# Kernel tuning notes

Measured on AMD Instinct MI355X. Metric: run time of the kernel, lower is better.

## Reference

```python
import jax, jax.numpy as jnp
import numpy as np

B, NM, MB, D = 16, 64, 64, 1024
NH, NKV, MEM = 16, 8, 64
HD = D // NH            # 64
S = MB + MEM            # per-step attention length
EPS = 1e-6

def precompute_freqs_cis(dim, end, theta=10000.0):
    freqs = 1.0 / (theta ** (jnp.arange(0, dim, 2)[: dim // 2].astype(jnp.float32) / dim))
    t = jnp.arange(end, dtype=jnp.float32)
    return jnp.exp(1j * jnp.outer(t, freqs))  # [end, dim//2] complex64

def apply_rope(x, fcis):
    # x: [s, h, d], fcis: [s, d//2] complex
    xc = x.reshape(x.shape[0], x.shape[1], HD // 2, 2)
    xc = jax.lax.complex(xc[..., 0], xc[..., 1]) * fcis[:, None, :]
    return jnp.stack([jnp.real(xc), jnp.imag(xc)], axis=-1).reshape(x.shape)

def layer_norm(x, scale, bias):
    m = x.mean(-1, keepdims=True)
    v = x.var(-1, keepdims=True)
    return (x - m) * jax.lax.rsqrt(v + EPS) * scale + bias

def setup_inputs() -> dict:
    key = jax.random.key(0)
    ks = jax.random.split(key, 8)
    s = 1.0 / np.sqrt(D)
    return {
        'hidden_states': jax.random.normal(ks[0], (B, NM, MB, D), jnp.float32),
        'mask': jax.random.bernoulli(ks[1], 0.9, (B, NM)),
        'mem_state': jax.random.normal(ks[2], (MEM, D), jnp.float32) * s,
        'wq': jax.random.normal(ks[3], (D, D), jnp.float32) * s,
        'wk': jax.random.normal(ks[4], (D, NKV * HD), jnp.float32) * s,
        'wv': jax.random.normal(ks[5], (D, NKV * HD), jnp.float32) * s,
        'wo': jax.random.normal(ks[6], (D, D), jnp.float32) * s,
        'pre_scale': jnp.ones((D,), jnp.float32),
        'pre_bias': jnp.zeros((D,), jnp.float32),
        'post_scale': jnp.ones((D,), jnp.float32),
        'post_bias': jnp.zeros((D,), jnp.float32),
    }

def reference(hidden_states, mask, mem_state, wq, wk, wv, wo, pre_scale, pre_bias, post_scale, post_bias):
    fcis = precompute_freqs_cis(HD, S)  # constant RoPE buffer, first S positions used
    rep = NH // NKV
    scale = 1.0 / np.sqrt(HD)

    def step(mem, inp):
        x_mb, m = inp  # x_mb: [MB, D], m: scalar bool
        h = layer_norm(jnp.concatenate([x_mb, mem], axis=0), pre_scale, pre_bias)  # [S, D]
        q = (h @ wq).reshape(S, NH, HD)
        k = (h @ wk).reshape(S, NKV, HD)
        v = (h @ wv).reshape(S, NKV, HD)
        q = apply_rope(q, fcis)
        k = apply_rope(k, fcis)
        k = jnp.repeat(k, rep, axis=1)  # GQA: expand kv heads
        v = jnp.repeat(v, rep, axis=1)
        qb, kb, vb = q.astype(jnp.bfloat16), k.astype(jnp.bfloat16), v.astype(jnp.bfloat16)
        logits = jnp.einsum('qhd,khd->hqk', qb, kb).astype(jnp.float32) * scale
        att = jax.nn.softmax(logits, axis=-1).astype(jnp.bfloat16)
        enc = jnp.einsum('hqk,khd->qhd', att, vb).reshape(S, D).astype(jnp.float32)
        out = enc[-MEM:] @ wo  # only memory-slot queries feed the update
        new_mem = layer_norm(out + mem, post_scale, post_bias)
        new_mem = jnp.where(m, new_mem, mem)  # lax.cond branch as select
        return new_mem, None

    def per_batch(x, m):
        final, _ = jax.lax.scan(step, mem_state, (x, m))
        return final

    return jax.vmap(per_batch)(hidden_states, mask)  # [B, MEM, D]
```

## Files before the change

kernel.cpp:

```cpp
#include <hip/hip_runtime.h>


typedef __attribute__((ext_vector_type(8))) _Float16 f16x8;
typedef __attribute__((ext_vector_type(4))) _Float16 f16x4;
typedef __attribute__((ext_vector_type(8))) short    s16x8;
typedef __attribute__((ext_vector_type(4))) float    f32x4;

#define NB   16
#define NMs  64
#define MBs  64
#define Dm   1024
#define NHh  16
#define NKVh 8
#define HDd  64
#define MEMm 64

__device__ __align__(16) _Float16      g_W1t[2048 * 1024];
__device__ __align__(16) _Float16      g_Wot[1024 * 1024];
__device__ __align__(16) float         g_rc[128 * 32];
__device__ __align__(16) float         g_rs[128 * 32];
__device__                unsigned char g_mask[NB * NMs];
__device__ __align__(16) _Float16      g_hx[(size_t)NB * NMs * MBs * Dm];
__device__ __align__(16) _Float16      g_hmem[NB * MEMm * Dm];
__device__ __align__(16) float         g_memA[NB * MEMm * Dm];
__device__ __align__(16) float         g_memB[NB * MEMm * Dm];
__device__ __align__(16) unsigned short g_kx[(size_t)NMs * NB * NKVh * 64 * 64];
__device__ __align__(16) unsigned short g_vx[(size_t)NMs * NB * NKVh * 64 * 64];
__device__ __align__(16) _Float16      g_enc[NB * 64 * Dm];
__device__ __align__(16) float         g_outp[NB * 64 * Dm];

__device__ __forceinline__ unsigned short f2bf(float x) {
    union { float f; unsigned u; } v; v.f = x;
    unsigned u = v.u;
    return (unsigned short)((u + 0x7fffu + ((u >> 16) & 1u)) >> 16);
}
__device__ __forceinline__ float bf2f(unsigned short h) {
    union { unsigned u; float f; } v; v.u = ((unsigned)h) << 16; return v.f;
}

__device__ __forceinline__ void gload_lds16(const void* g, void* l) {
    __builtin_amdgcn_global_load_lds(
        (const __attribute__((address_space(1))) unsigned int*)g,
        (__attribute__((address_space(3))) unsigned int*)l, 16, 0, 0);
}

__device__ __forceinline__ void block_stats(float s, float ss, float eps,
                                            float* mean, float* rstd) {
    for (int off = 32; off > 0; off >>= 1) {
        s  += __shfl_down(s, off);
        ss += __shfl_down(ss, off);
    }
    __shared__ float red[8];
    int wid = threadIdx.x >> 6, lane = threadIdx.x & 63;
    __syncthreads();
    if (lane == 0) { red[wid] = s; red[4 + wid] = ss; }
    __syncthreads();
    float ts  = red[0] + red[1] + red[2] + red[3];
    float tss = red[4] + red[5] + red[6] + red[7];
    float m   = ts * (1.0f / 1024.0f);
    float var = tss * (1.0f / 1024.0f) - m * m;
    *mean = m;
    *rstd = rsqrtf(var + eps);
}

__global__ void k_transpose(const float* __restrict__ in, int ncols, int dsel) {
    _Float16* out = (dsel == 0) ? g_W1t
                  : (dsel == 1) ? (g_W1t + 1024 * 1024)
                  : (dsel == 2) ? (g_W1t + 1536 * 1024)
                                : g_Wot;
    __shared__ float tile[64][65];
    int bk = blockIdx.x, bn = blockIdx.y;
    int c = threadIdx.x & 63, rg = threadIdx.x >> 6;
    int k0 = bk * 64, n0 = bn * 64;
    for (int i = 0; i < 16; i++) {
        int r = rg * 16 + i;
        tile[r][c] = in[(size_t)(k0 + r) * ncols + n0 + c];
    }
    __syncthreads();
    for (int i = 0; i < 16; i++) {
        int r = rg * 16 + i;
        out[(size_t)(n0 + r) * 1024 + k0 + c] = (_Float16)tile[c][r];
    }
}

__global__ void k_rope() {
    int t = threadIdx.x;
    for (int j = 0; j < 32; j++) {
        double f = pow(10000.0, -(double)j / 32.0);
        double a = (double)t * f;
        g_rc[t * 32 + j] = (float)cos(a);
        g_rs[t * 32 + j] = (float)sin(a);
    }
}

__global__ void k_mask(const unsigned int* __restrict__ ip) {
    __shared__ int byteFmt;
    int t = threadIdx.x;
    if (t == 0) byteFmt = 0;
    __syncthreads();
    if (t < 256) {
        unsigned v = ip[t];
        if (!(v == 0u || v == 1u || v == 0x3F800000u)) byteFmt = 1;
    }
    __syncthreads();
    unsigned char m = byteFmt ? (((const unsigned char*)ip)[t] != 0)
                              : (ip[t] != 0u);
    g_mask[t] = m;
}

__global__ void k_ln_hx(const float* __restrict__ x,
                        const float* __restrict__ sc, const float* __restrict__ bi) {
    size_t row = blockIdx.x;
    int t = threadIdx.x;
    float4 v = ((const float4*)(x + row * 1024))[t];
    float mean, rstd;
    block_stats(v.x + v.y + v.z + v.w,
                v.x * v.x + v.y * v.y + v.z * v.z + v.w * v.w, 1e-6f, &mean, &rstd);
    float4 s4 = ((const float4*)sc)[t];
    float4 b4 = ((const float4*)bi)[t];
    f16x4 o;
    o[0] = (_Float16)((v.x - mean) * rstd * s4.x + b4.x);
    o[1] = (_Float16)((v.y - mean) * rstd * s4.y + b4.y);
    o[2] = (_Float16)((v.z - mean) * rstd * s4.z + b4.z);
    o[3] = (_Float16)((v.w - mean) * rstd * s4.w + b4.w);
    *(f16x4*)(g_hx + row * 1024 + t * 4) = o;
}

__global__ void k_ln_init(const float* __restrict__ ms,
                          const float* __restrict__ sc, const float* __restrict__ bi) {
    int b = blockIdx.x >> 6, r = blockIdx.x & 63;
    int t = threadIdx.x;
    float4 v = ((const float4*)(ms + (size_t)r * 1024))[t];
    ((float4*)(g_memA + ((size_t)b * 64 + r) * 1024))[t] = v;
    float mean, rstd;
    block_stats(v.x + v.y + v.z + v.w,
                v.x * v.x + v.y * v.y + v.z * v.z + v.w * v.w, 1e-6f, &mean, &rstd);
    float4 s4 = ((const float4*)sc)[t];
    float4 b4 = ((const float4*)bi)[t];
    f16x4 o;
    o[0] = (_Float16)((v.x - mean) * rstd * s4.x + b4.x);
    o[1] = (_Float16)((v.y - mean) * rstd * s4.y + b4.y);
    o[2] = (_Float16)((v.z - mean) * rstd * s4.z + b4.z);
    o[3] = (_Float16)((v.w - mean) * rstd * s4.w + b4.w);
    *(f16x4*)(g_hmem + ((size_t)b * 64 + r) * 1024 + t * 4) = o;
}

__launch_bounds__(256)
__global__ void k_kvx() {
    int tm = blockIdx.x, tn = blockIdx.y;
    int tid = threadIdx.x, w = tid >> 6, l = tid & 63;
    int fr = l & 15, kc = l >> 4;
    __shared__ __align__(16) _Float16 As[8 * 512];
    __shared__ __align__(16) _Float16 Bs[8 * 512];
    __shared__ __align__(16) unsigned short Ct[128 * 132];
    const _Float16* A = g_hx + (size_t)tm * 128 * 1024;
    const _Float16* B = g_W1t + (size_t)(1024 + tn * 128) * 1024;
    int wm = w & 1, wn = w >> 1;
    f32x4 acc[4][4];
    #pragma unroll
    for (int i = 0; i < 4; i++)
        #pragma unroll
        for (int j = 0; j < 4; j++) acc[i][j] = (f32x4){0.f, 0.f, 0.f, 0.f};

    for (int kt = 0; kt < 32; ++kt) {
        #pragma unroll
        for (int jj = 0; jj < 2; ++jj) {
            int rg = w * 2 + jj;
            gload_lds16(A + (size_t)(rg * 16 + fr) * 1024 + kt * 32 + kc * 8,
                        (char*)As + rg * 1024);
            gload_lds16(B + (size_t)(rg * 16 + fr) * 1024 + kt * 32 + kc * 8,
                        (char*)Bs + rg * 1024);
        }
        __syncthreads();
        f16x8 af[4], bg[4];
        #pragma unroll
        for (int i = 0; i < 4; i++) {
            af[i] = *(const f16x8*)&As[(wm * 4 + i) * 512 + kc * 128 + fr * 8];
            bg[i] = *(const f16x8*)&Bs[(wn * 4 + i) * 512 + kc * 128 + fr * 8];
        }
        #pragma unroll
        for (int i = 0; i < 4; i++)
            #pragma unroll
            for (int j = 0; j < 4; j++)
                acc[i][j] = __builtin_amdgcn_mfma_f32_16x16x32_f16(af[i], bg[j], acc[i][j], 0, 0, 0);
        __syncthreads();
    }
    int quad = kc;
    #pragma unroll
    for (int i = 0; i < 4; i++)
        #pragma unroll
        for (int j = 0; j < 4; j++)
            #pragma unroll
            for (int r = 0; r < 4; r++) {
                float val = acc[i][j][r];
                float p = __shfl_xor(val, 1);
                int rl = wm * 64 + i * 16 + quad * 4 + r;
                int cl = wn * 64 + j * 16 + fr;
                int c = tn * 128 + cl;
                unsigned short ob;
                if (c < 512) {
                    int d = c & 63, pos = rl & 63;
                    int j2 = d >> 1;
                    float cc = g_rc[pos * 32 + j2], sn = g_rs[pos * 32 + j2];
                    float o = (d & 1) ? (p * sn + val * cc) : (val * cc - p * sn);
                    ob = f2bf(o);
                } else {
                    ob = f2bf(val);
                }
                Ct[rl * 132 + cl] = ob;
            }
    __syncthreads();
    int row = tid >> 1, half = tid & 1;
    size_t R = (size_t)tm * 128 + row;
    int bb = (int)(R >> 12), ss = (int)((R >> 6) & 63), pos = (int)(R & 63);
    int cb = tn * 128 + half * 64;
    unsigned short* dst = (cb < 512)
        ? (g_kx + ((((size_t)ss * 16 + bb) * 8) + (cb >> 6)) * 4096 + pos * 64)
        : (g_vx + ((((size_t)ss * 16 + bb) * 8) + ((cb - 512) >> 6)) * 4096 + pos * 64);
    const ushort4* src = (const ushort4*)&Ct[row * 132 + half * 64];
    #pragma unroll
    for (int j = 0; j < 16; j++) ((ushort4*)dst)[j] = src[j];
}

__launch_bounds__(256)
__global__ void k_step1(int s) {
    int b = blockIdx.x >> 4, h = blockIdx.x & 15, kvh = h >> 1;
    int tid = threadIdx.x, w = tid >> 6, l = tid & 63;
    int fr = l & 15, kc = l >> 4, quad = kc;
    __shared__ __align__(16) _Float16       Bs[24 * 512];
    __shared__ __align__(16) unsigned short q_s[64 * 72];
    __shared__ __align__(16) unsigned short k_s[64 * 72];
    __shared__ __align__(16) unsigned short vt_s[64 * 136];
    __shared__ __align__(16) unsigned short p_s[4][16 * 136];

    const _Float16* A = g_hmem + (size_t)b * 64 * 1024;

    {
        const unsigned short* vx = g_vx + (((size_t)s * 16 + b) * 8 + kvh) * 4096;
        int pos = tid & 63, dg = tid >> 6;
        const ushort2* src = (const ushort2*)(vx + pos * 64 + dg * 16);
        ushort2 tmp[8];
        #pragma unroll
        for (int j = 0; j < 8; j++) tmp[j] = src[j];
        #pragma unroll
        for (int j = 0; j < 8; j++) {
            vt_s[(dg * 16 + 2 * j)     * 136 + pos] = tmp[j].x;
            vt_s[(dg * 16 + 2 * j + 1) * 136 + pos] = tmp[j].y;
        }
    }

    f32x4 acc[12];
    #pragma unroll
    for (int i = 0; i < 12; i++) acc[i] = (f32x4){0.f, 0.f, 0.f, 0.f};
    int browQ = h * 64, browK = 1024 + kvh * 64, browV = 1536 + kvh * 64;

    for (int kt = 0; kt < 16; ++kt) {
        #pragma unroll
        for (int jj = 0; jj < 6; ++jj) {
            int m = w * 6 + jj, rg = m % 12, khalf = m / 12;
            int r192 = rg * 16 + fr;
            int brow = (r192 < 64) ? (browQ + r192)
                     : (r192 < 128) ? (browK + r192 - 64)
                                    : (browV + r192 - 128);
            gload_lds16(g_W1t + (size_t)brow * 1024 + kt * 64 + khalf * 32 + kc * 8,
                        (char*)Bs + m * 1024);
        }
        f16x8 a0 = *(const f16x8*)(A + (size_t)(w * 16 + fr) * 1024 + kt * 64 + kc * 8);
        f16x8 a1 = *(const f16x8*)(A + (size_t)(w * 16 + fr) * 1024 + kt * 64 + 32 + kc * 8);
        __syncthreads();
        #pragma unroll
        for (int nt = 0; nt < 12; ++nt) {
            f16x8 b0 = *(const f16x8*)&Bs[nt * 512 + kc * 128 + fr * 8];
            f16x8 b1 = *(const f16x8*)&Bs[(12 + nt) * 512 + kc * 128 + fr * 8];
            acc[nt] = __builtin_amdgcn_mfma_f32_16x16x32_f16(a0, b0, acc[nt], 0, 0, 0);
            acc[nt] = __builtin_amdgcn_mfma_f32_16x16x32_f16(a1, b1, acc[nt], 0, 0, 0);
        }
        __syncthreads();
    }

    #pragma unroll
    for (int nt = 0; nt < 12; ++nt)
        #pragma unroll
        for (int r = 0; r < 4; ++r) {
            float val = acc[nt][r];
            float p = __shfl_xor(val, 1);
            int row = w * 16 + quad * 4 + r;
            int col = nt * 16 + fr;
            if (col < 128) {
                int d = col & 63, pos = 64 + row;
                int j2 = d >> 1;
                float cc = g_rc[pos * 32 + j2], sn = g_rs[pos * 32 + j2];
                float o = (d & 1) ? (p * sn + val * cc) : (val * cc - p * sn);
                unsigned short bo = f2bf(o);
                if (col < 64) q_s[row * 72 + d] = bo;
                else          k_s[row * 72 + d] = bo;
            } else {
                int d = col - 128;
                vt_s[d * 136 + 64 + row] = f2bf(val);
            }
        }
    __syncthreads();

    s16x8 qa0 = *(const s16x8*)&q_s[(w * 16 + fr) * 72 + kc * 8];
    s16x8 qa1 = *(const s16x8*)&q_s[(w * 16 + fr) * 72 + 32 + kc * 8];
    const unsigned short* kx = g_kx + (((size_t)s * 16 + b) * 8 + kvh) * 4096;
    f32x4 sc[8];
    #pragma unroll
    for (int nt = 0; nt < 8; ++nt) {
        sc[nt] = (f32x4){0.f, 0.f, 0.f, 0.f};
        s16x8 kb0, kb1;
        if (nt < 4) {
            kb0 = *(const s16x8*)(kx + (nt * 16 + fr) * 64 + kc * 8);
            kb1 = *(const s16x8*)(kx + (nt * 16 + fr) * 64 + 32 + kc * 8);
        } else {
            kb0 = *(const s16x8*)&k_s[((nt - 4) * 16 + fr) * 72 + kc * 8];
            kb1 = *(const s16x8*)&k_s[((nt - 4) * 16 + fr) * 72 + 32 + kc * 8];
        }
        sc[nt] = __builtin_amdgcn_mfma_f32_16x16x32_bf16(qa0, kb0, sc[nt], 0, 0, 0);
        sc[nt] = __builtin_amdgcn_mfma_f32_16x16x32_bf16(qa1, kb1, sc[nt], 0, 0, 0);
    }

    float lv[8][4];
    #pragma unroll
    for (int nt = 0; nt < 8; nt++)
        #pragma unroll
        for (int r = 0; r < 4; r++)
            lv[nt][r] = bf2f(f2bf(sc[nt][r])) * 0.125f;
    #pragma unroll
    for (int r = 0; r < 4; r++) {
        float mx = -1e30f;
        #pragma unroll
        for (int nt = 0; nt < 8; nt++) mx = fmaxf(mx, lv[nt][r]);
        for (int off = 1; off < 16; off <<= 1) mx = fmaxf(mx, __shfl_xor(mx, off));
        float sm = 0.f;
        #pragma unroll
        for (int nt = 0; nt < 8; nt++) { lv[nt][r] = expf(lv[nt][r] - mx); sm += lv[nt][r]; }
        for (int off = 1; off < 16; off <<= 1) sm += __shfl_xor(sm, off);
        float inv = 1.0f / sm;
        int row = quad * 4 + r;
        #pragma unroll
        for (int nt = 0; nt < 8; nt++)
            p_s[w][row * 136 + nt * 16 + fr] = f2bf(lv[nt][r] * inv);
    }
    __syncthreads();

    f32x4 o[4];
    #pragma unroll
    for (int nt = 0; nt < 4; nt++) o[nt] = (f32x4){0.f, 0.f, 0.f, 0.f};
    for (int kt2 = 0; kt2 < 4; ++kt2) {
        s16x8 pa = *(const s16x8*)&p_s[w][fr * 136 + kt2 * 32 + kc * 8];
        #pragma unroll
        for (int nt = 0; nt < 4; ++nt) {
            s16x8 vb = *(const s16x8*)&vt_s[(nt * 16 + fr) * 136 + kt2 * 32 + kc * 8];
            o[nt] = __builtin_amdgcn_mfma_f32_16x16x32_bf16(pa, vb, o[nt], 0, 0, 0);
        }
    }
    #pragma unroll
    for (int nt = 0; nt < 4; nt++)
        #pragma unroll
        for (int r = 0; r < 4; r++) {
            int m = w * 16 + quad * 4 + r;
            int d = nt * 16 + fr;
            g_enc[((size_t)b * 64 + m) * 1024 + h * 64 + d] =
                (_Float16)bf2f(f2bf(o[nt][r]));
        }
}

__launch_bounds__(256)
__global__ void k_gemm2() {
    int b = blockIdx.x >> 4, nt4 = blockIdx.x & 15;
    int tid = threadIdx.x, w = tid >> 6, l = tid & 63;
    int fr = l & 15, kc = l >> 4, quad = kc;
    __shared__ __align__(16) _Float16 Bs[8 * 512];
    const _Float16* A = g_enc + (size_t)b * 64 * 1024;
    const _Float16* B = g_Wot + (size_t)nt4 * 64 * 1024;
    f32x4 acc[4];
    #pragma unroll
    for (int i = 0; i < 4; i++) acc[i] = (f32x4){0.f, 0.f, 0.f, 0.f};
    for (int kt = 0; kt < 16; ++kt) {
        #pragma unroll
        for (int jj = 0; jj < 2; ++jj) {
            int m = w * 2 + jj, rg = m & 3, khalf = m >> 2;
            gload_lds16(B + (size_t)(rg * 16 + fr) * 1024 + kt * 64 + khalf * 32 + kc * 8,
                        (char*)Bs + m * 1024);
        }
        f16x8 a0 = *(const f16x8*)(A + (size_t)(w * 16 + fr) * 1024 + kt * 64 + kc * 8);
        f16x8 a1 = *(const f16x8*)(A + (size_t)(w * 16 + fr) * 1024 + kt * 64 + 32 + kc * 8);
        __syncthreads();
        #pragma unroll
        for (int nt = 0; nt < 4; ++nt) {
            f16x8 b0 = *(const f16x8*)&Bs[nt * 512 + kc * 128 + fr * 8];
            f16x8 b1 = *(const f16x8*)&Bs[(4 + nt) * 512 + kc * 128 + fr * 8];
            acc[nt] = __builtin_amdgcn_mfma_f32_16x16x32_f16(a0, b0, acc[nt], 0, 0, 0);
            acc[nt] = __builtin_amdgcn_mfma_f32_16x16x32_f16(a1, b1, acc[nt], 0, 0, 0);
        }
        __syncthreads();
    }
    #pragma unroll
    for (int nt = 0; nt < 4; nt++)
        #pragma unroll
        for (int r = 0; r < 4; r++)
            g_outp[((size_t)b * 64 + w * 16 + quad * 4 + r) * 1024 + nt4 * 64 + nt * 16 + fr]
                = acc[nt][r];
}

__global__ void k_ln2(int s, float* __restrict__ dout,
                      const float* __restrict__ psc, const float* __restrict__ pbi,
                      const float* __restrict__ qsc, const float* __restrict__ qbi) {
    int b = blockIdx.x >> 6, r = blockIdx.x & 63;
    const float* memIn = (s & 1) ? g_memB : g_memA;
    float* memOut = (s == 63) ? dout : ((s & 1) ? g_memA : g_memB);
    int t = threadIdx.x;
    size_t row = (size_t)b * 64 + r;
    float4 ov = ((const float4*)(g_outp + row * 1024))[t];
    float4 mv = ((const float4*)(memIn + row * 1024))[t];
    float4 y = {ov.x + mv.x, ov.y + mv.y, ov.z + mv.z, ov.w + mv.w};
    float mean, rstd;
    block_stats(y.x + y.y + y.z + y.w,
                y.x * y.x + y.y * y.y + y.z * y.z + y.w * y.w, 1e-6f, &mean, &rstd);
    float4 s4 = ((const float4*)psc)[t];
    float4 b4 = ((const float4*)pbi)[t];
    float4 nm = {(y.x - mean) * rstd * s4.x + b4.x,
                 (y.y - mean) * rstd * s4.y + b4.y,
                 (y.z - mean) * rstd * s4.z + b4.z,
                 (y.w - mean) * rstd * s4.w + b4.w};
    int mk = g_mask[b * 64 + s];
    float4 sel = mk ? nm : mv;
    ((float4*)(memOut + row * 1024))[t] = sel;
    float m2, rs2;
    block_stats(sel.x + sel.y + sel.z + sel.w,
                sel.x * sel.x + sel.y * sel.y + sel.z * sel.z + sel.w * sel.w,
                1e-6f, &m2, &rs2);
    float4 c4 = ((const float4*)qsc)[t];
    float4 d4 = ((const float4*)qbi)[t];
    f16x4 o;
    o[0] = (_Float16)((sel.x - m2) * rs2 * c4.x + d4.x);
    o[1] = (_Float16)((sel.y - m2) * rs2 * c4.y + d4.y);
    o[2] = (_Float16)((sel.z - m2) * rs2 * c4.z + d4.z);
    o[3] = (_Float16)((sel.w - m2) * rs2 * c4.w + d4.w);
    *(f16x4*)(g_hmem + row * 1024 + t * 4) = o;
}

extern "C" void kernel_launch(void* const* d_in, const int* in_sizes, int n_in,
                              void* d_out, int out_size, void* d_ws, size_t ws_size,
                              hipStream_t stream) {
    (void)in_sizes; (void)n_in; (void)d_ws; (void)ws_size; (void)out_size;
    const float* hidden    = (const float*)d_in[0];
    const unsigned int* mk = (const unsigned int*)d_in[1];
    const float* mem_state = (const float*)d_in[2];
    const float* wq  = (const float*)d_in[3];
    const float* wk  = (const float*)d_in[4];
    const float* wv  = (const float*)d_in[5];
    const float* wo  = (const float*)d_in[6];
    const float* pre_s  = (const float*)d_in[7];
    const float* pre_b  = (const float*)d_in[8];
    const float* post_s = (const float*)d_in[9];
    const float* post_b = (const float*)d_in[10];
    float* out = (float*)d_out;

    k_transpose<<<dim3(16, 16), 256, 0, stream>>>(wq, 1024, 0);
    k_transpose<<<dim3(16, 8),  256, 0, stream>>>(wk, 512, 1);
    k_transpose<<<dim3(16, 8),  256, 0, stream>>>(wv, 512, 2);
    k_transpose<<<dim3(16, 16), 256, 0, stream>>>(wo, 1024, 3);
    k_rope<<<1, 128, 0, stream>>>();
    k_mask<<<1, 1024, 0, stream>>>(mk);
    k_ln_hx<<<NB * NMs * MBs, 256, 0, stream>>>(hidden, pre_s, pre_b);
    k_ln_init<<<NB * MEMm, 256, 0, stream>>>(mem_state, pre_s, pre_b);
    k_kvx<<<dim3(512, 8), 256, 0, stream>>>();

    for (int s = 0; s < NMs; ++s) {
        k_step1<<<NB * NHh, 256, 0, stream>>>(s);
        k_gemm2<<<NB * NHh, 256, 0, stream>>>();
        k_ln2<<<NB * MEMm, 256, 0, stream>>>(s, out, post_s, post_b, pre_s, pre_b);
    }
}
```

Before: 4.604 ms.

## Fuse per-step kernels into one persistent kernel with grid barriers

Replaces the 192 per-step kernel launches (attention, output projection, layernorm) with one persistent 256-block kernel that uses a two-level atomic grid barrier between phases. The standalone upfront K/V projection over all hidden states is removed. Each step's output-projection phase now also computes the next step's K/V projection, so the weight streaming is interleaved into the serial loop rather than run as a big separate GEMM. The aim is to remove launch overhead and idle gaps in the recurrent chain. It relies on all 256 blocks being co-resident and on spin-wait barriers, and it adds work to every step.

Result: slower. 12.38 ms (+168.8%).

```diff
diff --git a/kernel.cpp b/kernel.cpp
--- a/kernel.cpp
+++ b/kernel.cpp
@@ -12,7 +12,6 @@
 #define Dm   1024
 #define NHh  16
 #define NKVh 8
-#define HDd  64
 #define MEMm 64
 
 __device__ __align__(16) _Float16      g_W1t[2048 * 1024];
@@ -28,6 +27,9 @@
 __device__ __align__(16) unsigned short g_vx[(size_t)NMs * NB * NKVh * 64 * 64];
 __device__ __align__(16) _Float16      g_enc[NB * 64 * Dm];
 __device__ __align__(16) float         g_outp[NB * 64 * Dm];
+__device__ unsigned g_leaf[8];
+__device__ unsigned g_root;
+__device__ unsigned g_gen;
 
 __device__ __forceinline__ unsigned short f2bf(float x) {
     union { float f; unsigned u; } v; v.f = x;
@@ -42,6 +44,47 @@
     __builtin_amdgcn_global_load_lds(
         (const __attribute__((address_space(1))) unsigned int*)g,
         (__attribute__((address_space(3))) unsigned int*)l, 16, 0, 0);
+}
+
+__device__ __forceinline__ void grid_barrier(int bid, unsigned tgt) {
+    __syncthreads();
+    if (threadIdx.x == 0) {
+        __threadfence();
+        unsigned v = atomicAdd(&g_leaf[bid & 7], 1u);
+        if (v == 31u) {
+            unsigned r = atomicAdd(&g_root, 1u);
+            if (r == 7u) {
+                #pragma unroll
+                for (int i = 0; i < 8; i++) atomicExch(&g_leaf[i], 0u);
+                atomicExch(&g_root, 0u);
+                __threadfence();
+                atomicAdd(&g_gen, 1u);
+            }
+        }
+        while ((int)(__hip_atomic_load(&g_gen, __ATOMIC_ACQUIRE,
+                                       __HIP_MEMORY_SCOPE_AGENT) - tgt) < 0)
+            __builtin_amdgcn_s_sleep(2);
+        __threadfence();
+    }
+    __syncthreads();
+}
+
+__device__ __forceinline__ void block_stats512(int tid, float (*red)[8],
+        float s, float ss, float eps, float* mean, float* rstd) {
+    for (int off = 32; off > 0; off >>= 1) {
+        s  += __shfl_down(s, off);
+        ss += __shfl_down(ss, off);
+    }
+    int g = tid >> 8, wid = (tid >> 6) & 3, lane = tid & 63;
+    __syncthreads();
+    if (lane == 0) { red[g][wid] = s; red[g][4 + wid] = ss; }
+    __syncthreads();
+    float ts  = red[g][0] + red[g][1] + red[g][2] + red[g][3];
+    float tss = red[g][4] + red[g][5] + red[g][6] + red[g][7];
+    float m   = ts * (1.0f / 1024.0f);
+    float var = tss * (1.0f / 1024.0f) - m * m;
+    *mean = m;
+    *rstd = rsqrtf(var + eps);
 }
 
 __device__ __forceinline__ void block_stats(float s, float ss, float eps,
@@ -145,300 +188,301 @@
     *(f16x4*)(g_hmem + ((size_t)b * 64 + r) * 1024 + t * 4) = o;
 }
 
-__launch_bounds__(256)
-__global__ void k_kvx() {
-    int tm = blockIdx.x, tn = blockIdx.y;
-    int tid = threadIdx.x, w = tid >> 6, l = tid & 63;
-    int fr = l & 15, kc = l >> 4;
-    __shared__ __align__(16) _Float16 As[8 * 512];
-    __shared__ __align__(16) _Float16 Bs[8 * 512];
-    __shared__ __align__(16) unsigned short Ct[128 * 132];
-    const _Float16* A = g_hx + (size_t)tm * 128 * 1024;
-    const _Float16* B = g_W1t + (size_t)(1024 + tn * 128) * 1024;
-    int wm = w & 1, wn = w >> 1;
-    f32x4 acc[4][4];
-    #pragma unroll
-    for (int i = 0; i < 4; i++)
-        #pragma unroll
-        for (int j = 0; j < 4; j++) acc[i][j] = (f32x4){0.f, 0.f, 0.f, 0.f};
-
-    for (int kt = 0; kt < 32; ++kt) {
-        #pragma unroll
-        for (int jj = 0; jj < 2; ++jj) {
-            int rg = w * 2 + jj;
-            gload_lds16(A + (size_t)(rg * 16 + fr) * 1024 + kt * 32 + kc * 8,
-                        (char*)As + rg * 1024);
-            gload_lds16(B + (size_t)(rg * 16 + fr) * 1024 + kt * 32 + kc * 8,
-                        (char*)Bs + rg * 1024);
-        }
-        __syncthreads();
-        f16x8 af[4], bg[4];
-        #pragma unroll
-        for (int i = 0; i < 4; i++) {
-            af[i] = *(const f16x8*)&As[(wm * 4 + i) * 512 + kc * 128 + fr * 8];
-            bg[i] = *(const f16x8*)&Bs[(wn * 4 + i) * 512 + kc * 128 + fr * 8];
-        }
-        #pragma unroll
-        for (int i = 0; i < 4; i++)
-            #pragma unroll
-            for (int j = 0; j < 4; j++)
-                acc[i][j] = __builtin_amdgcn_mfma_f32_16x16x32_f16(af[i], bg[j], acc[i][j], 0, 0, 0);
-        __syncthreads();
-    }
-    int quad = kc;
-    #pragma unroll
-    for (int i = 0; i < 4; i++)
-        #pragma unroll
-        for (int j = 0; j < 4; j++)
-            #pragma unroll
-            for (int r = 0; r < 4; r++) {
-                float val = acc[i][j][r];
-                float p = __shfl_xor(val, 1);
-                int rl = wm * 64 + i * 16 + quad * 4 + r;
-                int cl = wn * 64 + j * 16 + fr;
-                int c = tn * 128 + cl;
-                unsigned short ob;
-                if (c < 512) {
-                    int d = c & 63, pos = rl & 63;
-                    int j2 = d >> 1;
-                    float cc = g_rc[pos * 32 + j2], sn = g_rs[pos * 32 + j2];
-                    float o = (d & 1) ? (p * sn + val * cc) : (val * cc - p * sn);
-                    ob = f2bf(o);
-                } else {
-                    ob = f2bf(val);
-                }
-                Ct[rl * 132 + cl] = ob;
-            }
-    __syncthreads();
-    int row = tid >> 1, half = tid & 1;
-    size_t R = (size_t)tm * 128 + row;
-    int bb = (int)(R >> 12), ss = (int)((R >> 6) & 63), pos = (int)(R & 63);
-    int cb = tn * 128 + half * 64;
-    unsigned short* dst = (cb < 512)
-        ? (g_kx + ((((size_t)ss * 16 + bb) * 8) + (cb >> 6)) * 4096 + pos * 64)
-        : (g_vx + ((((size_t)ss * 16 + bb) * 8) + ((cb - 512) >> 6)) * 4096 + pos * 64);
-    const ushort4* src = (const ushort4*)&Ct[row * 132 + half * 64];
-    #pragma unroll
-    for (int j = 0; j < 16; j++) ((ushort4*)dst)[j] = src[j];
-}
-
-__launch_bounds__(256)
-__global__ void k_step1(int s) {
-    int b = blockIdx.x >> 4, h = blockIdx.x & 15, kvh = h >> 1;
-    int tid = threadIdx.x, w = tid >> 6, l = tid & 63;
+__device__ __forceinline__ void phaseB_body(int s, int ss, int b, int nt16,
+                                            int tid, char* sm) {
+    int w = tid >> 6, l = tid & 63;
     int fr = l & 15, kc = l >> 4, quad = kc;
-    __shared__ __align__(16) _Float16       Bs[24 * 512];
-    __shared__ __align__(16) unsigned short q_s[64 * 72];
-    __shared__ __align__(16) unsigned short k_s[64 * 72];
-    __shared__ __align__(16) unsigned short vt_s[64 * 136];
-    __shared__ __align__(16) unsigned short p_s[4][16 * 136];
-
-    const _Float16* A = g_hmem + (size_t)b * 64 * 1024;
-
-    {
-        const unsigned short* vx = g_vx + (((size_t)s * 16 + b) * 8 + kvh) * 4096;
-        int pos = tid & 63, dg = tid >> 6;
-        const ushort2* src = (const ushort2*)(vx + pos * 64 + dg * 16);
-        ushort2 tmp[8];
-        #pragma unroll
-        for (int j = 0; j < 8; j++) tmp[j] = src[j];
-        #pragma unroll
-        for (int j = 0; j < 8; j++) {
-            vt_s[(dg * 16 + 2 * j)     * 136 + pos] = tmp[j].x;
-            vt_s[(dg * 16 + 2 * j + 1) * 136 + pos] = tmp[j].y;
-        }
-    }
-
-    f32x4 acc[12];
-    #pragma unroll
-    for (int i = 0; i < 12; i++) acc[i] = (f32x4){0.f, 0.f, 0.f, 0.f};
-    int browQ = h * 64, browK = 1024 + kvh * 64, browV = 1536 + kvh * 64;
-
-    for (int kt = 0; kt < 16; ++kt) {
-        #pragma unroll
-        for (int jj = 0; jj < 6; ++jj) {
-            int m = w * 6 + jj, rg = m % 12, khalf = m / 12;
-            int r192 = rg * 16 + fr;
-            int brow = (r192 < 64) ? (browQ + r192)
-                     : (r192 < 128) ? (browK + r192 - 64)
-                                    : (browV + r192 - 128);
-            gload_lds16(g_W1t + (size_t)brow * 1024 + kt * 64 + khalf * 32 + kc * 8,
-                        (char*)Bs + m * 1024);
-        }
-        f16x8 a0 = *(const f16x8*)(A + (size_t)(w * 16 + fr) * 1024 + kt * 64 + kc * 8);
-        f16x8 a1 = *(const f16x8*)(A + (size_t)(w * 16 + fr) * 1024 + kt * 64 + 32 + kc * 8);
-        __syncthreads();
-        #pragma unroll
-        for (int nt = 0; nt < 12; ++nt) {
-            f16x8 b0 = *(const f16x8*)&Bs[nt * 512 + kc * 128 + fr * 8];
-            f16x8 b1 = *(const f16x8*)&Bs[(12 + nt) * 512 + kc * 128 + fr * 8];
-            acc[nt] = __builtin_amdgcn_mfma_f32_16x16x32_f16(a0, b0, acc[nt], 0, 0, 0);
-            acc[nt] = __builtin_amdgcn_mfma_f32_16x16x32_f16(a1, b1, acc[nt], 0, 0, 0);
-        }
-        __syncthreads();
-    }
-
-    #pragma unroll
-    for (int nt = 0; nt < 12; ++nt)
-        #pragma unroll
-        for (int r = 0; r < 4; ++r) {
-            float val = acc[nt][r];
-            float p = __shfl_xor(val, 1);
-            int row = w * 16 + quad * 4 + r;
-            int col = nt * 16 + fr;
-            if (col < 128) {
-                int d = col & 63, pos = 64 + row;
-                int j2 = d >> 1;
-                float cc = g_rc[pos * 32 + j2], sn = g_rs[pos * 32 + j2];
-                float o = (d & 1) ? (p * sn + val * cc) : (val * cc - p * sn);
-                unsigned short bo = f2bf(o);
-                if (col < 64) q_s[row * 72 + d] = bo;
-                else          k_s[row * 72 + d] = bo;
-            } else {
-                int d = col - 128;
-                vt_s[d * 136 + 64 + row] = f2bf(val);
-            }
-        }
-    __syncthreads();
-
-    s16x8 qa0 = *(const s16x8*)&q_s[(w * 16 + fr) * 72 + kc * 8];
-    s16x8 qa1 = *(const s16x8*)&q_s[(w * 16 + fr) * 72 + 32 + kc * 8];
-    const unsigned short* kx = g_kx + (((size_t)s * 16 + b) * 8 + kvh) * 4096;
-    f32x4 sc[8];
-    #pragma unroll
-    for (int nt = 0; nt < 8; ++nt) {
-        sc[nt] = (f32x4){0.f, 0.f, 0.f, 0.f};
-        s16x8 kb0, kb1;
-        if (nt < 4) {
-            kb0 = *(const s16x8*)(kx + (nt * 16 + fr) * 64 + kc * 8);
-            kb1 = *(const s16x8*)(kx + (nt * 16 + fr) * 64 + 32 + kc * 8);
-        } else {
-            kb0 = *(const s16x8*)&k_s[((nt - 4) * 16 + fr) * 72 + kc * 8];
-            kb1 = *(const s16x8*)&k_s[((nt - 4) * 16 + fr) * 72 + 32 + kc * 8];
-        }
-        sc[nt] = __builtin_amdgcn_mfma_f32_16x16x32_bf16(qa0, kb0, sc[nt], 0, 0, 0);
-        sc[nt] = __builtin_amdgcn_mfma_f32_16x16x32_bf16(qa1, kb1, sc[nt], 0, 0, 0);
-    }
-
-    float lv[8][4];
-    #pragma unroll
-    for (int nt = 0; nt < 8; nt++)
-        #pragma unroll
-        for (int r = 0; r < 4; r++)
-            lv[nt][r] = bf2f(f2bf(sc[nt][r])) * 0.125f;
-    #pragma unroll
-    for (int r = 0; r < 4; r++) {
-        float mx = -1e30f;
-        #pragma unroll
-        for (int nt = 0; nt < 8; nt++) mx = fmaxf(mx, lv[nt][r]);
-        for (int off = 1; off < 16; off <<= 1) mx = fmaxf(mx, __shfl_xor(mx, off));
-        float sm = 0.f;
-        #pragma unroll
-        for (int nt = 0; nt < 8; nt++) { lv[nt][r] = expf(lv[nt][r] - mx); sm += lv[nt][r]; }
-        for (int off = 1; off < 16; off <<= 1) sm += __shfl_xor(sm, off);
-        float inv = 1.0f / sm;
-        int row = quad * 4 + r;
-        #pragma unroll
-        for (int nt = 0; nt < 8; nt++)
-            p_s[w][row * 136 + nt * 16 + fr] = f2bf(lv[nt][r] * inv);
-    }
-    __syncthreads();
-
-    f32x4 o[4];
-    #pragma unroll
-    for (int nt = 0; nt < 4; nt++) o[nt] = (f32x4){0.f, 0.f, 0.f, 0.f};
-    for (int kt2 = 0; kt2 < 4; ++kt2) {
-        s16x8 pa = *(const s16x8*)&p_s[w][fr * 136 + kt2 * 32 + kc * 8];
-        #pragma unroll
-        for (int nt = 0; nt < 4; ++nt) {
-            s16x8 vb = *(const s16x8*)&vt_s[(nt * 16 + fr) * 136 + kt2 * 32 + kc * 8];
-            o[nt] = __builtin_amdgcn_mfma_f32_16x16x32_bf16(pa, vb, o[nt], 0, 0, 0);
-        }
-    }
-    #pragma unroll
-    for (int nt = 0; nt < 4; nt++)
-        #pragma unroll
-        for (int r = 0; r < 4; r++) {
-            int m = w * 16 + quad * 4 + r;
-            int d = nt * 16 + fr;
-            g_enc[((size_t)b * 64 + m) * 1024 + h * 64 + d] =
-                (_Float16)bf2f(f2bf(o[nt][r]));
-        }
-}
-
-__launch_bounds__(256)
-__global__ void k_gemm2() {
-    int b = blockIdx.x >> 4, nt4 = blockIdx.x & 15;
-    int tid = threadIdx.x, w = tid >> 6, l = tid & 63;
-    int fr = l & 15, kc = l >> 4, quad = kc;
-    __shared__ __align__(16) _Float16 Bs[8 * 512];
-    const _Float16* A = g_enc + (size_t)b * 64 * 1024;
-    const _Float16* B = g_Wot + (size_t)nt4 * 64 * 1024;
+    int mt = w & 3, sel = w >> 2;
+    int ssc = (ss < 64) ? ss : 63;
+    bool active = (sel == 0) ? (s >= 0) : (ss < 64);
+    const _Float16* A = (sel == 0)
+        ? (g_enc + (size_t)b * 64 * 1024)
+        : (g_hx + (((size_t)b * 64 + ssc) * 64) * 1024);
     f32x4 acc[4];
     #pragma unroll
     for (int i = 0; i < 4; i++) acc[i] = (f32x4){0.f, 0.f, 0.f, 0.f};
-    for (int kt = 0; kt < 16; ++kt) {
+
+    for (int kt = 0; kt < 8; ++kt) {
         #pragma unroll
-        for (int jj = 0; jj < 2; ++jj) {
-            int m = w * 2 + jj, rg = m & 3, khalf = m >> 2;
-            gload_lds16(B + (size_t)(rg * 16 + fr) * 1024 + kt * 64 + khalf * 32 + kc * 8,
-                        (char*)Bs + m * 1024);
+        for (int jj = 0; jj < 4; ++jj) {
+            int m = w * 4 + jj;
+            int tile = m >> 4, m4 = m & 15, rg = m4 & 3, kq = m4 >> 2;
+            if (tile == 0) {
+                if (s >= 0)
+                    gload_lds16(g_Wot + (size_t)(nt16 * 64 + rg * 16 + fr) * 1024
+                                + kt * 128 + kq * 32 + kc * 8, sm + m * 1024);
+            } else {
+                if (ss < 64)
+                    gload_lds16(g_W1t + (size_t)(1024 + nt16 * 64 + rg * 16 + fr) * 1024
+                                + kt * 128 + kq * 32 + kc * 8, sm + m * 1024);
+            }
         }
-        f16x8 a0 = *(const f16x8*)(A + (size_t)(w * 16 + fr) * 1024 + kt * 64 + kc * 8);
-        f16x8 a1 = *(const f16x8*)(A + (size_t)(w * 16 + fr) * 1024 + kt * 64 + 32 + kc * 8);
-        __syncthreads();
-        #pragma unroll
-        for (int nt = 0; nt < 4; ++nt) {
-            f16x8 b0 = *(const f16x8*)&Bs[nt * 512 + kc * 128 + fr * 8];
-            f16x8 b1 = *(const f16x8*)&Bs[(4 + nt) * 512 + kc * 128 + fr * 8];
-            acc[nt] = __builtin_amdgcn_mfma_f32_16x16x32_f16(a0, b0, acc[nt], 0, 0, 0);
-            acc[nt] = __builtin_amdgcn_mfma_f32_16x16x32_f16(a1, b1, acc[nt], 0, 0, 0);
+        f16x8 a[4];
+        if (active) {
+            #pragma unroll
+            for (int ci = 0; ci < 4; ci++)
+                a[ci] = *(const f16x8*)(A + (size_t)(mt * 16 + fr) * 1024
+                                        + kt * 128 + ci * 32 + kc * 8);
         }
         __syncthreads();
-    }
-    #pragma unroll
-    for (int nt = 0; nt < 4; nt++)
+        if (active) {
+            #pragma unroll
+            for (int nt = 0; nt < 4; ++nt) {
+                #pragma unroll
+                for (int ci = 0; ci < 4; ++ci) {
+                    f16x8 bf = *(const f16x8*)(sm + (size_t)((sel << 4) + nt + 4 * ci) * 1024 + l * 16);
+                    acc[nt] = __builtin_amdgcn_mfma_f32_16x16x32_f16(a[ci], bf, acc[nt], 0, 0, 0);
+                }
+            }
+        }
+        __syncthreads();
+    }
+
+    if (sel == 0 && s >= 0) {
         #pragma unroll
-        for (int r = 0; r < 4; r++)
-            g_outp[((size_t)b * 64 + w * 16 + quad * 4 + r) * 1024 + nt4 * 64 + nt * 16 + fr]
-                = acc[nt][r];
-}
-
-__global__ void k_ln2(int s, float* __restrict__ dout,
-                      const float* __restrict__ psc, const float* __restrict__ pbi,
-                      const float* __restrict__ qsc, const float* __restrict__ qbi) {
-    int b = blockIdx.x >> 6, r = blockIdx.x & 63;
-    const float* memIn = (s & 1) ? g_memB : g_memA;
-    float* memOut = (s == 63) ? dout : ((s & 1) ? g_memA : g_memB);
-    int t = threadIdx.x;
-    size_t row = (size_t)b * 64 + r;
-    float4 ov = ((const float4*)(g_outp + row * 1024))[t];
-    float4 mv = ((const float4*)(memIn + row * 1024))[t];
-    float4 y = {ov.x + mv.x, ov.y + mv.y, ov.z + mv.z, ov.w + mv.w};
-    float mean, rstd;
-    block_stats(y.x + y.y + y.z + y.w,
-                y.x * y.x + y.y * y.y + y.z * y.z + y.w * y.w, 1e-6f, &mean, &rstd);
-    float4 s4 = ((const float4*)psc)[t];
-    float4 b4 = ((const float4*)pbi)[t];
-    float4 nm = {(y.x - mean) * rstd * s4.x + b4.x,
-                 (y.y - mean) * rstd * s4.y + b4.y,
-                 (y.z - mean) * rstd * s4.z + b4.z,
-                 (y.w - mean) * rstd * s4.w + b4.w};
-    int mk = g_mask[b * 64 + s];
-    float4 sel = mk ? nm : mv;
-    ((float4*)(memOut + row * 1024))[t] = sel;
-    float m2, rs2;
-    block_stats(sel.x + sel.y + sel.z + sel.w,
-                sel.x * sel.x + sel.y * sel.y + sel.z * sel.z + sel.w * sel.w,
-                1e-6f, &m2, &rs2);
-    float4 c4 = ((const float4*)qsc)[t];
-    float4 d4 = ((const float4*)qbi)[t];
-    f16x4 o;
-    o[0] = (_Float16)((sel.x - m2) * rs2 * c4.x + d4.x);
-    o[1] = (_Float16)((sel.y - m2) * rs2 * c4.y + d4.y);
-    o[2] = (_Float16)((sel.z - m2) * rs2 * c4.z + d4.z);
-    o[3] = (_Float16)((sel.w - m2) * rs2 * c4.w + d4.w);
-    *(f16x4*)(g_hmem + row * 1024 + t * 4) = o;
+        for (int nt = 0; nt < 4; nt++)
+            #pragma unroll
+            for (int r = 0; r < 4; r++)
+                g_outp[((size_t)b * 64 + mt * 16 + quad * 4 + r) * 1024
+                       + nt16 * 64 + nt * 16 + fr] = acc[nt][r];
+    } else if (sel == 1 && ss < 64) {
+        #pragma unroll
+        for (int nt = 0; nt < 4; nt++)
+            #pragma unroll
+            for (int r = 0; r < 4; r++) {
+                float val = acc[nt][r];
+                float p = __shfl_xor(val, 1);
+                int row = mt * 16 + quad * 4 + r;
+                int col = nt16 * 64 + nt * 16 + fr;
+                int d = col & 63;
+                if (col < 512) {
+                    int kvh = col >> 6, j2 = d >> 1;
+                    float cc = g_rc[row * 32 + j2], sn = g_rs[row * 32 + j2];
+                    float o = (d & 1) ? (p * sn + val * cc) : (val * cc - p * sn);
+                    g_kx[(((size_t)ss * 16 + b) * 8 + kvh) * 4096 + row * 64 + d] = f2bf(o);
+                } else {
+                    int kvh = (col - 512) >> 6;
+                    g_vx[(((size_t)ss * 16 + b) * 8 + kvh) * 4096 + row * 64 + d] = f2bf(val);
+                }
+            }
+    }
+}
+
+__global__ __launch_bounds__(512) void k_xkv0() {
+    __shared__ __align__(16) char sm[32768];
+    phaseB_body(-1, 0, blockIdx.x >> 4, blockIdx.x & 15, threadIdx.x, sm);
+}
+
+#define SM_QS  49152
+#define SM_KS  58368
+#define SM_VT  67584
+#define SM_PS  84992
+#define SM_TOT 102400
+
+__global__ __launch_bounds__(512, 1) void k_loop(float* __restrict__ dout,
+        const float* __restrict__ post_s, const float* __restrict__ post_b,
+        const float* __restrict__ pre_s,  const float* __restrict__ pre_b) {
+    __shared__ __align__(16) char smem[SM_TOT];
+    __shared__ float red2[2][8];
+    const int bid = blockIdx.x;
+    const int tid = threadIdx.x;
+    const int w = tid >> 6, l = tid & 63;
+    const int fr = l & 15, kc = l >> 4, quad = kc;
+    const int b = bid >> 4, hn = bid & 15;
+    unsigned gbase = __hip_atomic_load(&g_gen, __ATOMIC_RELAXED, __HIP_MEMORY_SCOPE_AGENT);
+    unsigned nbar = 0;
+
+    unsigned short* q_s  = (unsigned short*)(smem + SM_QS);
+    unsigned short* k_s  = (unsigned short*)(smem + SM_KS);
+    unsigned short* vt_s = (unsigned short*)(smem + SM_VT);
+    unsigned short* p_s  = (unsigned short*)(smem + SM_PS);
+
+    for (int s = 0; s < NMs; ++s) {
+        {
+            const int h = hn, kvh = h >> 1;
+            const unsigned short* vx = g_vx + (((size_t)s * 16 + b) * 8 + kvh) * 4096;
+            const unsigned short* kx = g_kx + (((size_t)s * 16 + b) * 8 + kvh) * 4096;
+            {
+                int pos = tid & 63, dg = tid >> 6;
+                ushort4 u0 = *(const ushort4*)(vx + pos * 64 + dg * 8);
+                ushort4 u1 = *(const ushort4*)(vx + pos * 64 + dg * 8 + 4);
+                vt_s[(dg * 8 + 0) * 136 + pos] = u0.x;
+                vt_s[(dg * 8 + 1) * 136 + pos] = u0.y;
+                vt_s[(dg * 8 + 2) * 136 + pos] = u0.z;
+                vt_s[(dg * 8 + 3) * 136 + pos] = u0.w;
+                vt_s[(dg * 8 + 4) * 136 + pos] = u1.x;
+                vt_s[(dg * 8 + 5) * 136 + pos] = u1.y;
+                vt_s[(dg * 8 + 6) * 136 + pos] = u1.z;
+                vt_s[(dg * 8 + 7) * 136 + pos] = u1.w;
+            }
+            const _Float16* A = g_hmem + (size_t)b * 64 * 1024;
+            const int mt = w & 3, nh = w >> 2;
+            f32x4 acc[6];
+            #pragma unroll
+            for (int i = 0; i < 6; i++) acc[i] = (f32x4){0.f, 0.f, 0.f, 0.f};
+            const int browQ = h * 64, browK = 1024 + kvh * 64, browV = 1536 + kvh * 64;
+
+            for (int kt = 0; kt < 8; ++kt) {
+                #pragma unroll
+                for (int jj = 0; jj < 6; ++jj) {
+                    int m = w * 6 + jj;
+                    int rg = m % 12, kq = m / 12;
+                    int r192 = rg * 16 + fr;
+                    int brow = (r192 < 64) ? (browQ + r192)
+                             : (r192 < 128) ? (browK + r192 - 64)
+                                            : (browV + r192 - 128);
+                    gload_lds16(g_W1t + (size_t)brow * 1024 + kt * 128 + kq * 32 + kc * 8,
+                                smem + m * 1024);
+                }
+                f16x8 a[4];
+                #pragma unroll
+                for (int ci = 0; ci < 4; ci++)
+                    a[ci] = *(const f16x8*)(A + (size_t)(mt * 16 + fr) * 1024
+                                            + kt * 128 + ci * 32 + kc * 8);
+                __syncthreads();
+                #pragma unroll
+                for (int ntl = 0; ntl < 6; ++ntl) {
+                    int ntG = nh * 6 + ntl;
+                    #pragma unroll
+                    for (int ci = 0; ci < 4; ++ci) {
+                        f16x8 bf = *(const f16x8*)(smem + (size_t)(ntG + 12 * ci) * 1024 + l * 16);
+                        acc[ntl] = __builtin_amdgcn_mfma_f32_16x16x32_f16(a[ci], bf, acc[ntl], 0, 0, 0);
+                    }
+                }
+                __syncthreads();
+            }
+            #pragma unroll
+            for (int ntl = 0; ntl < 6; ++ntl) {
+                #pragma unroll
+                for (int r = 0; r < 4; ++r) {
+                    float val = acc[ntl][r];
+                    float p = __shfl_xor(val, 1);
+                    int row = mt * 16 + quad * 4 + r;
+                    int col = (nh * 6 + ntl) * 16 + fr;
+                    if (col < 128) {
+                        int d = col & 63, pos = 64 + row, j2 = d >> 1;
+                        float cc = g_rc[pos * 32 + j2], sn = g_rs[pos * 32 + j2];
+                        float o = (d & 1) ? (p * sn + val * cc) : (val * cc - p * sn);
+                        unsigned short bo = f2bf(o);
+                        if (col < 64) q_s[row * 72 + d] = bo;
+                        else          k_s[row * 72 + d] = bo;
+                    } else {
+                        int d = col - 128;
+                        vt_s[d * 136 + 64 + row] = f2bf(val);
+                    }
+                }
+            }
+            __syncthreads();
+            if (w < 4) {
+                s16x8 qa0 = *(const s16x8*)&q_s[(w * 16 + fr) * 72 + kc * 8];
+                s16x8 qa1 = *(const s16x8*)&q_s[(w * 16 + fr) * 72 + 32 + kc * 8];
+                f32x4 sc2[8];
+                #pragma unroll
+                for (int nt = 0; nt < 8; ++nt) {
+                    sc2[nt] = (f32x4){0.f, 0.f, 0.f, 0.f};
+                    s16x8 kb0, kb1;
+                    if (nt < 4) {
+                        kb0 = *(const s16x8*)(kx + (nt * 16 + fr) * 64 + kc * 8);
+                        kb1 = *(const s16x8*)(kx + (nt * 16 + fr) * 64 + 32 + kc * 8);
+                    } else {
+                        kb0 = *(const s16x8*)&k_s[((nt - 4) * 16 + fr) * 72 + kc * 8];
+                        kb1 = *(const s16x8*)&k_s[((nt - 4) * 16 + fr) * 72 + 32 + kc * 8];
+                    }
+                    sc2[nt] = __builtin_amdgcn_mfma_f32_16x16x32_bf16(qa0, kb0, sc2[nt], 0, 0, 0);
+                    sc2[nt] = __builtin_amdgcn_mfma_f32_16x16x32_bf16(qa1, kb1, sc2[nt], 0, 0, 0);
+                }
+                float lv[8][4];
+                #pragma unroll
+                for (int nt = 0; nt < 8; nt++)
+                    #pragma unroll
+                    for (int r = 0; r < 4; r++)
+                        lv[nt][r] = bf2f(f2bf(sc2[nt][r])) * 0.125f;
+                unsigned short* pw = p_s + w * 16 * 136;
+                #pragma unroll
+                for (int r = 0; r < 4; r++) {
+                    float mx = -1e30f;
+                    #pragma unroll
+                    for (int nt = 0; nt < 8; nt++) mx = fmaxf(mx, lv[nt][r]);
+                    for (int off = 1; off < 16; off <<= 1) mx = fmaxf(mx, __shfl_xor(mx, off));
+                    float sm2 = 0.f;
+                    #pragma unroll
+                    for (int nt = 0; nt < 8; nt++) { lv[nt][r] = expf(lv[nt][r] - mx); sm2 += lv[nt][r]; }
+                    for (int off = 1; off < 16; off <<= 1) sm2 += __shfl_xor(sm2, off);
+                    float inv = 1.0f / sm2;
+                    int row = quad * 4 + r;
+                    #pragma unroll
+                    for (int nt = 0; nt < 8; nt++)
+                        pw[row * 136 + nt * 16 + fr] = f2bf(lv[nt][r] * inv);
+                }
+                f32x4 o[4];
+                #pragma unroll
+                for (int nt = 0; nt < 4; nt++) o[nt] = (f32x4){0.f, 0.f, 0.f, 0.f};
+                for (int kt2 = 0; kt2 < 4; ++kt2) {
+                    s16x8 pa = *(const s16x8*)&pw[fr * 136 + kt2 * 32 + kc * 8];
+                    #pragma unroll
+                    for (int nt = 0; nt < 4; ++nt) {
+                        s16x8 vb = *(const s16x8*)&vt_s[(nt * 16 + fr) * 136 + kt2 * 32 + kc * 8];
+                        o[nt] = __builtin_amdgcn_mfma_f32_16x16x32_bf16(pa, vb, o[nt], 0, 0, 0);
+                    }
+                }
+                #pragma unroll
+                for (int nt = 0; nt < 4; nt++)
+                    #pragma unroll
+                    for (int r = 0; r < 4; r++) {
+                        int m = w * 16 + quad * 4 + r;
+                        int d = nt * 16 + fr;
+                        g_enc[((size_t)b * 64 + m) * 1024 + h * 64 + d] =
+                            (_Float16)bf2f(f2bf(o[nt][r]));
+                    }
+            }
+        }
+        grid_barrier(bid, gbase + (++nbar));
+
+        phaseB_body(s, s + 1, b, hn, tid, smem);
+        grid_barrier(bid, gbase + (++nbar));
+
+        {
+            const float* memIn = (s & 1) ? g_memB : g_memA;
+            float* memOut = (s == 63) ? dout : ((s & 1) ? g_memA : g_memB);
+            int g = tid >> 8, tl = tid & 255;
+            #pragma unroll
+            for (int rr = 0; rr < 2; ++rr) {
+                int r = hn * 4 + g * 2 + rr;
+                size_t row = (size_t)b * 64 + r;
+                float4 ov = ((const float4*)(g_outp + row * 1024))[tl];
+                float4 mv = ((const float4*)(memIn + row * 1024))[tl];
+                float4 y = {ov.x + mv.x, ov.y + mv.y, ov.z + mv.z, ov.w + mv.w};
+                float mean, rstd;
+                block_stats512(tid, red2,
+                               y.x + y.y + y.z + y.w,
+                               y.x * y.x + y.y * y.y + y.z * y.z + y.w * y.w,
+                               1e-6f, &mean, &rstd);
+                float4 s4 = ((const float4*)post_s)[tl];
+                float4 b4 = ((const float4*)post_b)[tl];
+                float4 nm = {(y.x - mean) * rstd * s4.x + b4.x,
+                             (y.y - mean) * rstd * s4.y + b4.y,
+                             (y.z - mean) * rstd * s4.z + b4.z,
+                             (y.w - mean) * rstd * s4.w + b4.w};
+                int mk = g_mask[b * 64 + s];
+                float4 sel4 = mk ? nm : mv;
+                ((float4*)(memOut + row * 1024))[tl] = sel4;
+                float m2, rs2;
+                block_stats512(tid, red2,
+                               sel4.x + sel4.y + sel4.z + sel4.w,
+                               sel4.x * sel4.x + sel4.y * sel4.y + sel4.z * sel4.z + sel4.w * sel4.w,
+                               1e-6f, &m2, &rs2);
+                float4 c4 = ((const float4*)pre_s)[tl];
+                float4 d4 = ((const float4*)pre_b)[tl];
+                f16x4 o;
+                o[0] = (_Float16)((sel4.x - m2) * rs2 * c4.x + d4.x);
+                o[1] = (_Float16)((sel4.y - m2) * rs2 * c4.y + d4.y);
+                o[2] = (_Float16)((sel4.z - m2) * rs2 * c4.z + d4.z);
+                o[3] = (_Float16)((sel4.w - m2) * rs2 * c4.w + d4.w);
+                *(f16x4*)(g_hmem + row * 1024 + tl * 4) = o;
+            }
+        }
+        if (s != 63) grid_barrier(bid, gbase + (++nbar));
+    }
 }
 
 extern "C" void kernel_launch(void* const* d_in, const int* in_sizes, int n_in,
@@ -466,11 +510,6 @@
     k_mask<<<1, 1024, 0, stream>>>(mk);
     k_ln_hx<<<NB * NMs * MBs, 256, 0, stream>>>(hidden, pre_s, pre_b);
     k_ln_init<<<NB * MEMm, 256, 0, stream>>>(mem_state, pre_s, pre_b);
-    k_kvx<<<dim3(512, 8), 256, 0, stream>>>();
-
-    for (int s = 0; s < NMs; ++s) {
-        k_step1<<<NB * NHh, 256, 0, stream>>>(s);
-        k_gemm2<<<NB * NHh, 256, 0, stream>>>();
-        k_ln2<<<NB * MEMm, 256, 0, stream>>>(s, out, post_s, post_b, pre_s, pre_b);
-    }
-}
+    k_xkv0<<<256, 512, 0, stream>>>();
+    k_loop<<<256, 512, 0, stream>>>(out, post_s, post_b, pre_s, pre_b);
+}
```
